# Kernel optimization log

Hardware: AMD Instinct MI355X
Metric: run time of the kernel (lower is better)

## Reference

```python
import jax, jax.numpy as jnp
import numpy as np

NUM_ITERATIONS = 10


def _nearest_neighbor(src, tgt):
    # src: [B,N,3], tgt: [B,M,3] -> indices [B,N] of nearest tgt point per src point
    inner = -2.0 * jnp.einsum('bnd,bmd->bnm', src, tgt)            # [B,N,M]
    xx = jnp.sum(src * src, axis=2, keepdims=True)                  # [B,N,1]
    yy = jnp.sum(tgt * tgt, axis=2, keepdims=True).transpose(0, 2, 1)  # [B,1,M]
    distances = xx + inner + yy                                     # [B,N,M]
    return jnp.argmin(distances, axis=2)                            # [B,N]


def _compute_transformation(src, tgt):
    # src, tgt: [B,N,3] matched pairs -> rigid (R [B,3,3], t [B,3])
    N = src.shape[1]
    c_src = jnp.mean(src, axis=1, keepdims=True)                    # [B,1,3]
    c_tgt = jnp.mean(tgt, axis=1, keepdims=True)                    # [B,1,3]
    H = jnp.einsum('bnd,bne->bde', src - c_src, tgt - c_tgt) / N    # [B,3,3]
    U, S, Vh = jnp.linalg.svd(H, full_matrices=False)
    V = jnp.swapaxes(Vh, -1, -2)                                    # matches torch.svd's V
    R = V @ jnp.swapaxes(U, -1, -2)
    det = jnp.linalg.det(R)                                         # [B]
    sign = 1.0 - 2.0 * (det < 0).astype(src.dtype)                  # +1 or -1
    # torch code scales V[:, :, 2] (third column of V)
    V = V * jnp.concatenate([jnp.ones_like(sign)[:, None],
                             jnp.ones_like(sign)[:, None],
                             sign[:, None]], axis=1)[:, None, :]    # scale col 2
    R = V @ jnp.swapaxes(U, -1, -2)                                 # [B,3,3]
    t = c_tgt[:, 0, :] - jnp.einsum('bij,bj->bi', R, c_src[:, 0, :])  # [B,3]
    return R, t


def _icp(src, tgt):
    transformed_src = src
    R = None
    t = None
    for _ in range(NUM_ITERATIONS):
        indices = _nearest_neighbor(transformed_src, tgt)           # [B,N]
        matched_tgt = jnp.take_along_axis(tgt, indices[:, :, None], axis=1)  # [B,N,3]
        R, t = _compute_transformation(transformed_src, matched_tgt)
        # faithful to torch: x @ R + t (R applied on the right)
        transformed_src = jnp.einsum('bnd,bde->bne', transformed_src, R) + t[:, None, :]
    return R, t, transformed_src


def setup_inputs() -> dict:
    key = jax.random.key(0)
    k1, k2 = jax.random.split(key)
    src = jax.random.normal(k1, (4, 4096, 3), dtype=jnp.float32)
    tgt = jax.random.normal(k2, (4, 4096, 3), dtype=jnp.float32)
    return {"src": src, "tgt": tgt}


def reference(src, tgt):
    # Returns (est_R [B,3,3], est_t [B,3], transformed_source [B,N,3])
    return _icp(src, tgt)
```

## Files before the change

kernel.cpp:

```cpp
#include <hip/hip_runtime.h>
#include <math.h>

#define NB 4
#define NP 4096
#define MP 4096

typedef __bf16 bf16x8 __attribute__((ext_vector_type(8)));
typedef float  f32x16 __attribute__((ext_vector_type(16)));

static __device__ __forceinline__ unsigned short bh(float f) {
    unsigned u = __float_as_uint(f);
    unsigned r = (u + 0x7FFFu + ((u >> 16) & 1u)) >> 16;
    return (unsigned short)r;
}
static __device__ __forceinline__ float hf(unsigned short h) {
    return __uint_as_float(((unsigned)h) << 16);
}

static __device__ __forceinline__ float frcp(float x)  { return __builtin_amdgcn_rcpf(x); }
static __device__ __forceinline__ float frsq(float x)  { return __builtin_amdgcn_rsqf(x); }
static __device__ __forceinline__ float fsqrt(float x) { return __builtin_amdgcn_sqrtf(x); }

__device__ __forceinline__ void kabsch_f32(const float* s, float* RtL) {
    const float invN = 1.0f / (float)NP;
    float cs[3] = { s[0] * invN, s[1] * invN, s[2] * invN };
    float ct[3] = { s[3] * invN, s[4] * invN, s[5] * invN };
    float H[3][3];
    for (int d = 0; d < 3; ++d)
        for (int e = 0; e < 3; ++e)
            H[d][e] = s[6 + d * 3 + e] * invN - cs[d] * ct[e];

    float A[3][3];
    for (int i = 0; i < 3; ++i)
        for (int j = 0; j < 3; ++j)
            A[i][j] = H[0][i] * H[0][j] + H[1][i] * H[1][j] + H[2][i] * H[2][j];

    float V[3][3] = {{1, 0, 0}, {0, 1, 0}, {0, 0, 1}};
    for (int sweep = 0; sweep < 6; ++sweep) {
        float off = A[0][1] * A[0][1] + A[0][2] * A[0][2] + A[1][2] * A[1][2];
        if (off < 1e-16f) break;
        for (int pi = 0; pi < 3; ++pi) {
            const int p = (pi == 2) ? 1 : 0;
            const int q = (pi == 0) ? 1 : 2;
            float apq = A[p][q];
            if (fabsf(apq) < 1e-30f) continue;
            float theta = (A[q][q] - A[p][p]) * 0.5f * frcp(apq);
            float t = frcp(fabsf(theta) + fsqrt(1.0f + theta * theta));
            if (theta < 0.0f) t = -t;
            float cth = frsq(1.0f + t * t);
            float sth = t * cth;
            float App = A[p][p], Aqq = A[q][q];
            A[p][p] = App - t * apq;
            A[q][q] = Aqq + t * apq;
            A[p][q] = A[q][p] = 0.0f;
            const int r = 3 - p - q;
            float Apr = A[p][r], Aqr = A[q][r];
            A[p][r] = A[r][p] = cth * Apr - sth * Aqr;
            A[q][r] = A[r][q] = sth * Apr + cth * Aqr;
            for (int i = 0; i < 3; ++i) {
                float Vip = V[i][p], Viq = V[i][q];
                V[i][p] = cth * Vip - sth * Viq;
                V[i][q] = sth * Vip + cth * Viq;
            }
        }
    }
    float lam[3] = { A[0][0], A[1][1], A[2][2] };
    for (int i = 0; i < 2; ++i)
        for (int j = i + 1; j < 3; ++j)
            if (lam[j] > lam[i]) {
                float tl = lam[i]; lam[i] = lam[j]; lam[j] = tl;
                for (int k = 0; k < 3; ++k) {
                    float tv = V[k][i]; V[k][i] = V[k][j]; V[k][j] = tv;
                }
            }

    float U[3][3];
    for (int k = 0; k < 3; ++k) {
        float w0 = H[0][0] * V[0][k] + H[0][1] * V[1][k] + H[0][2] * V[2][k];
        float w1 = H[1][0] * V[0][k] + H[1][1] * V[1][k] + H[1][2] * V[2][k];
        float w2 = H[2][0] * V[0][k] + H[2][1] * V[1][k] + H[2][2] * V[2][k];
        float d2 = w0 * w0 + w1 * w1 + w2 * w2;
        if (d2 > 1e-40f) {
            float inr = frsq(d2);
            U[0][k] = w0 * inr; U[1][k] = w1 * inr; U[2][k] = w2 * inr;
        } else {
            U[0][k] = U[1][0] * U[2][1] - U[2][0] * U[1][1];
            U[1][k] = U[2][0] * U[0][1] - U[0][0] * U[2][1];
            U[2][k] = U[0][0] * U[1][1] - U[1][0] * U[0][1];
        }
    }

    float detH = H[0][0] * (H[1][1] * H[2][2] - H[1][2] * H[2][1])
               - H[0][1] * (H[1][0] * H[2][2] - H[1][2] * H[2][0])
               + H[0][2] * (H[1][0] * H[2][1] - H[1][1] * H[2][0]);
    float sgn = (detH < 0.0f) ? -1.0f : 1.0f;

    float R[3][3];
    for (int i = 0; i < 3; ++i)
        for (int j = 0; j < 3; ++j)
            R[i][j] = V[i][0] * U[j][0] + V[i][1] * U[j][1] + sgn * V[i][2] * U[j][2];
    float tv[3];
    for (int i = 0; i < 3; ++i)
        tv[i] = ct[i] - (R[i][0] * cs[0] + R[i][1] * cs[1] + R[i][2] * cs[2]);

    for (int i = 0; i < 3; ++i)
        for (int j = 0; j < 3; ++j)
            RtL[i * 3 + j] = R[i][j];
    for (int i = 0; i < 3; ++i) RtL[9 + i] = tv[i];
}

__global__ __launch_bounds__(256) void icp_init(const float* __restrict__ tgt,
                                                float4* __restrict__ tgt4,
                                                uint4* __restrict__ Bbuf) {
    const int t    = blockIdx.x * 256 + threadIdx.x;
    const int b    = t >> 13;
    const int rem  = t & 8191;
    const int tile = rem >> 6;
    const int lane = rem & 63;
    const int n    = lane & 31;
    const int h    = lane >> 5;
    const int gt   = b * MP + tile * 32 + n;

    float x = tgt[gt * 3 + 0];
    float y = tgt[gt * 3 + 1];
    float z = tgt[gt * 3 + 2];
    float wv = x * x + y * y + z * z;

    unsigned short xh = bh(x), xl = bh(x - hf(xh));
    unsigned short yh = bh(y), yl = bh(y - hf(yh));
    unsigned short zh = bh(z), zl = bh(z - hf(zh));
    unsigned short wh = bh(wv), wl = bh(wv - hf(wh));
    const unsigned short ONE = 0x3F80;

    unsigned short s0, s1, s2, s3, s4, s5, s6, s7;
    if (h == 0) { s0 = xh; s1 = xh; s2 = xl; s3 = xl;
                  s4 = yh; s5 = yh; s6 = yl; s7 = yl; }
    else        { s0 = zh; s1 = zh; s2 = zl; s3 = zl;
                  s4 = wh; s5 = wl; s6 = ONE; s7 = ONE; }
    uint4 u;
    u.x = (unsigned)s0 | ((unsigned)s1 << 16);
    u.y = (unsigned)s2 | ((unsigned)s3 << 16);
    u.z = (unsigned)s4 | ((unsigned)s5 << 16);
    u.w = (unsigned)s6 | ((unsigned)s7 << 16);
    Bbuf[t] = u;

    if (h == 0) tgt4[gt] = make_float4(x, y, z, wv);
}

__global__ __launch_bounds__(1024, 4) void icp_scan(
        const float* __restrict__ src,
        const float4* __restrict__ tgt4,
        const uint4* __restrict__ Bbuf,
        float* __restrict__ S,
        const float* __restrict__ pprev,
        float* __restrict__ pout,
        int first) {
    __shared__ unsigned CK[512];
    __shared__ float RtL[12];

    const int blk = blockIdx.x;
    const int b   = blk >> 6;
    const int g   = blk & 63;
    const int tid = threadIdx.x;
    const int w   = tid >> 6;
    const int l   = tid & 63;
    const int ts  = w & 1;
    const int tr  = w >> 1;
    const int gsrc = b * NP + g * 64 + l;

    const uint4* Bw = Bbuf + (b * 128 + tr * 16) * 64;
    uint4 fb[4];
    fb[0] = Bw[l];
    fb[1] = Bw[64 + l];
    fb[2] = Bw[128 + l];
    fb[3] = Bw[192 + l];

    const float* P = first ? src : S;
    float x0 = P[gsrc * 3 + 0];
    float y0 = P[gsrc * 3 + 1];
    float z0 = P[gsrc * 3 + 2];

    if (w == 0) {
        if (first) {
            if (l < 12) RtL[l] = (l == 0 || l == 4 || l == 8) ? 1.0f : 0.0f;
        } else {
            const float4* rp = (const float4*)(pprev + (b * 64 + l) * 16);
            float4 r0 = rp[0], r1 = rp[1], r2 = rp[2], r3 = rp[3];
            float sm[15] = { r0.x, r0.y, r0.z, r0.w, r1.x, r1.y, r1.z, r1.w,
                             r2.x, r2.y, r2.z, r2.w, r3.x, r3.y, r3.z };
            #pragma unroll
            for (int k = 0; k < 15; ++k) {
                float v = sm[k];
                v += __shfl_down(v, 32);
                v += __shfl_down(v, 16);
                v += __shfl_down(v, 8);
                v += __shfl_down(v, 4);
                v += __shfl_down(v, 2);
                v += __shfl_down(v, 1);
                sm[k] = v;
            }
            if (l == 0) kabsch_f32(sm, RtL);
        }
    }
    __syncthreads();

    float px = x0 * RtL[0] + y0 * RtL[3] + z0 * RtL[6] + RtL[9];
    float py = x0 * RtL[1] + y0 * RtL[4] + z0 * RtL[7] + RtL[10];
    float pz = x0 * RtL[2] + y0 * RtL[5] + z0 * RtL[8] + RtL[11];
    if (w == 1) {
        S[gsrc * 3 + 0] = px;
        S[gsrc * 3 + 1] = py;
        S[gsrc * 3 + 2] = pz;
    }

    const int h = l >> 5;
    union { unsigned short s[8]; bf16x8 v; } Af;
    {
        const int j3 = ts * 32 + (l & 31);
        float pxj = __shfl(px, j3);
        float pyj = __shfl(py, j3);
        float pzj = __shfl(pz, j3);
        float ax = -2.0f * pxj, ay = -2.0f * pyj, az = -2.0f * pzj;
        float qv = pxj * pxj + pyj * pyj + pzj * pzj + 1.0f;
        unsigned short axh = bh(ax), axl = bh(ax - hf(axh));
        unsigned short ayh = bh(ay), ayl = bh(ay - hf(ayh));
        unsigned short azh = bh(az), azl = bh(az - hf(azh));
        unsigned short qh  = bh(qv), ql  = bh(qv - hf(qh));
        const unsigned short ONE = 0x3F80;
        if (h == 0) {
            Af.s[0] = axh; Af.s[1] = axl; Af.s[2] = axh; Af.s[3] = axl;
            Af.s[4] = ayh; Af.s[5] = ayl; Af.s[6] = ayh; Af.s[7] = ayl;
        } else {
            Af.s[0] = azh; Af.s[1] = azl; Af.s[2] = azh; Af.s[3] = azl;
            Af.s[4] = ONE; Af.s[5] = ONE; Af.s[6] = qh;  Af.s[7] = ql;
        }
    }

    f32x16 zero;
    #pragma unroll
    for (int i = 0; i < 16; ++i) zero[i] = 0.0f;

    float best[16];
    #pragma unroll
    for (int r = 0; r < 16; ++r) best[r] = __uint_as_float(0x7F7FFFFFu);

    const int col = l & 31;

    #pragma unroll
    for (int t = 0; t < 16; ++t) {
        bf16x8 Bf = __builtin_bit_cast(bf16x8, fb[t & 3]);
        if (t < 12) fb[t & 3] = Bw[(t + 4) * 64 + l];
        f32x16 d16 = __builtin_amdgcn_mfma_f32_32x32x16_bf16(Af.v, Bf, zero,
                                                             0, 0, 0);
        const unsigned idxk = (unsigned)((tr * 16 + t) * 32 + col);
        #pragma unroll
        for (int r = 0; r < 16; ++r) {
            float key = __uint_as_float(
                (__float_as_uint(d16[r]) & 0xFFFFF000u) | idxk);
            best[r] = fminf(best[r], key);
        }
    }

    #pragma unroll
    for (int r = 0; r < 16; ++r) {
        float v = best[r];
        v = fminf(v, __shfl_xor(v, 1));
        v = fminf(v, __shfl_xor(v, 2));
        v = fminf(v, __shfl_xor(v, 4));
        v = fminf(v, __shfl_xor(v, 8));
        v = fminf(v, __shfl_xor(v, 16));
        best[r] = v;
    }
    if ((l & 31) == 0) {
        #pragma unroll
        for (int r = 0; r < 16; ++r) {
            const int row = (r & 3) + 8 * (r >> 2) + 4 * h;
            CK[tr * 64 + ts * 32 + row] = __float_as_uint(best[r]);
        }
    }
    __syncthreads();

    if (w == 0) {
        unsigned kb = CK[l];
        #pragma unroll
        for (int k = 1; k < 8; ++k) {
            unsigned kk = CK[k * 64 + l];
            kb = kk < kb ? kk : kb;
        }
        const int idx = kb & 0xFFF;
        float4 mt = tgt4[b * MP + idx];
        const float tx = mt.x, ty = mt.y, tz = mt.z;

        float v[15];
        v[0]  = px;      v[1]  = py;      v[2]  = pz;
        v[3]  = tx;      v[4]  = ty;      v[5]  = tz;
        v[6]  = px * tx; v[7]  = px * ty; v[8]  = px * tz;
        v[9]  = py * tx; v[10] = py * ty; v[11] = py * tz;
        v[12] = pz * tx; v[13] = pz * ty; v[14] = pz * tz;
        #pragma unroll
        for (int k = 0; k < 15; ++k) {
            float s = v[k];
            s += __shfl_down(s, 32);
            s += __shfl_down(s, 16);
            s += __shfl_down(s, 8);
            s += __shfl_down(s, 4);
            s += __shfl_down(s, 2);
            s += __shfl_down(s, 1);
            v[k] = s;
        }
        if (l == 0) {
            float* pp = pout + blk * 16;
            #pragma unroll
            for (int k = 0; k < 15; ++k) pp[k] = v[k];
        }
    }
}

__global__ __launch_bounds__(256) void icp_final(
        const float* __restrict__ S,
        const float* __restrict__ plast,
        float* __restrict__ out) {
    __shared__ float RtL[12];
    const int bk  = blockIdx.x;
    const int tid = threadIdx.x;
    const int gid = bk * 256 + tid;
    const int b   = gid >> 12;

    if (tid < 64) {
        const float4* rp = (const float4*)(plast + (b * 64 + tid) * 16);
        float4 r0 = rp[0], r1 = rp[1], r2 = rp[2], r3 = rp[3];
        float sm[15] = { r0.x, r0.y, r0.z, r0.w, r1.x, r1.y, r1.z, r1.w,
                         r2.x, r2.y, r2.z, r2.w, r3.x, r3.y, r3.z };
        #pragma unroll
        for (int k = 0; k < 15; ++k) {
            float v = sm[k];
            v += __shfl_down(v, 32);
            v += __shfl_down(v, 16);
            v += __shfl_down(v, 8);
            v += __shfl_down(v, 4);
            v += __shfl_down(v, 2);
            v += __shfl_down(v, 1);
            sm[k] = v;
        }
        if (tid == 0) kabsch_f32(sm, RtL);
    }
    __syncthreads();

    float x = S[gid * 3 + 0];
    float y = S[gid * 3 + 1];
    float z = S[gid * 3 + 2];
    out[48 + gid * 3 + 0] = x * RtL[0] + y * RtL[3] + z * RtL[6] + RtL[9];
    out[48 + gid * 3 + 1] = x * RtL[1] + y * RtL[4] + z * RtL[7] + RtL[10];
    out[48 + gid * 3 + 2] = x * RtL[2] + y * RtL[5] + z * RtL[8] + RtL[11];
    if ((bk & 15) == 0) {
        if (tid < 9) out[b * 9 + tid] = RtL[tid];
        if (tid < 3) out[36 + b * 3 + tid] = RtL[9 + tid];
    }
}

extern "C" void kernel_launch(void* const* d_in, const int* in_sizes, int n_in,
                              void* d_out, int out_size, void* d_ws, size_t ws_size,
                              hipStream_t stream) {
    const float* src = (const float*)d_in[0];
    const float* tgt = (const float*)d_in[1];
    float* out = (float*)d_out;

    float* W     = (float*)d_ws;
    float4* tgt4 = (float4*)W;
    uint4*  Bbuf = (uint4*)(W + 65536);
    float*  S    = W + 65536 + 131072;
    float*  pA   = S + 49152;
    float*  pB   = pA + 4096;
    float* bufs[2] = { pA, pB };

    icp_init<<<128, 256, 0, stream>>>(tgt, tgt4, Bbuf);
    for (int k = 0; k < 10; ++k) {
        icp_scan<<<256, 1024, 0, stream>>>(src, tgt4, Bbuf, S,
                                           bufs[(k + 1) & 1], bufs[k & 1],
                                           k == 0 ? 1 : 0);
    }
    icp_final<<<64, 256, 0, stream>>>(S, bufs[1], out);
}
```

Baseline: 173.5 us.

## Split scan into 512 blocks of 32 source points each with 8 warps

Measured after the change: 199.2 us. +14.8%, slower.

```diff
diff --git a/kernel.cpp b/kernel.cpp
--- a/kernel.cpp
+++ b/kernel.cpp
@@ -147,7 +147,7 @@
     if (h == 0) tgt4[gt] = make_float4(x, y, z, wv);
 }
 
-__global__ __launch_bounds__(1024, 4) void icp_scan(
+__global__ __launch_bounds__(512, 4) void icp_scan(
         const float* __restrict__ src,
         const float4* __restrict__ tgt4,
         const uint4* __restrict__ Bbuf,
@@ -155,20 +155,20 @@
         const float* __restrict__ pprev,
         float* __restrict__ pout,
         int first) {
-    __shared__ unsigned CK[512];
+    __shared__ unsigned CK[256];
     __shared__ float RtL[12];
 
     const int blk = blockIdx.x;
-    const int b   = blk >> 6;
-    const int g   = blk & 63;
+    const int b   = blk >> 7;
+    const int g   = blk & 127;
     const int tid = threadIdx.x;
     const int w   = tid >> 6;
     const int l   = tid & 63;
-    const int ts  = w & 1;
-    const int tr  = w >> 1;
-    const int gsrc = b * NP + g * 64 + l;
-
-    const uint4* Bw = Bbuf + (b * 128 + tr * 16) * 64;
+    const int m   = l & 31;
+    const int h   = l >> 5;
+    const int gsrc = b * NP + g * 32 + m;
+
+    const uint4* Bw = Bbuf + (b * 128 + w * 16) * 64;
     uint4 fb[4];
     fb[0] = Bw[l];
     fb[1] = Bw[64 + l];
@@ -184,10 +184,14 @@
         if (first) {
             if (l < 12) RtL[l] = (l == 0 || l == 4 || l == 8) ? 1.0f : 0.0f;
         } else {
-            const float4* rp = (const float4*)(pprev + (b * 64 + l) * 16);
-            float4 r0 = rp[0], r1 = rp[1], r2 = rp[2], r3 = rp[3];
-            float sm[15] = { r0.x, r0.y, r0.z, r0.w, r1.x, r1.y, r1.z, r1.w,
-                             r2.x, r2.y, r2.z, r2.w, r3.x, r3.y, r3.z };
+            const float4* rp0 = (const float4*)(pprev + (b * 128 + l) * 16);
+            const float4* rp1 = (const float4*)(pprev + (b * 128 + 64 + l) * 16);
+            float4 a0 = rp0[0], a1 = rp0[1], a2 = rp0[2], a3 = rp0[3];
+            float4 c0 = rp1[0], c1 = rp1[1], c2 = rp1[2], c3 = rp1[3];
+            float sm[15] = { a0.x + c0.x, a0.y + c0.y, a0.z + c0.z, a0.w + c0.w,
+                             a1.x + c1.x, a1.y + c1.y, a1.z + c1.z, a1.w + c1.w,
+                             a2.x + c2.x, a2.y + c2.y, a2.z + c2.z, a2.w + c2.w,
+                             a3.x + c3.x, a3.y + c3.y, a3.z + c3.z };
             #pragma unroll
             for (int k = 0; k < 15; ++k) {
                 float v = sm[k];
@@ -207,21 +211,16 @@
     float px = x0 * RtL[0] + y0 * RtL[3] + z0 * RtL[6] + RtL[9];
     float py = x0 * RtL[1] + y0 * RtL[4] + z0 * RtL[7] + RtL[10];
     float pz = x0 * RtL[2] + y0 * RtL[5] + z0 * RtL[8] + RtL[11];
-    if (w == 1) {
+    if (w == 1 && h == 0) {
         S[gsrc * 3 + 0] = px;
         S[gsrc * 3 + 1] = py;
         S[gsrc * 3 + 2] = pz;
     }
 
-    const int h = l >> 5;
     union { unsigned short s[8]; bf16x8 v; } Af;
     {
-        const int j3 = ts * 32 + (l & 31);
-        float pxj = __shfl(px, j3);
-        float pyj = __shfl(py, j3);
-        float pzj = __shfl(pz, j3);
-        float ax = -2.0f * pxj, ay = -2.0f * pyj, az = -2.0f * pzj;
-        float qv = pxj * pxj + pyj * pyj + pzj * pzj + 1.0f;
+        float ax = -2.0f * px, ay = -2.0f * py, az = -2.0f * pz;
+        float qv = px * px + py * py + pz * pz + 1.0f;
         unsigned short axh = bh(ax), axl = bh(ax - hf(axh));
         unsigned short ayh = bh(ay), ayl = bh(ay - hf(ayh));
         unsigned short azh = bh(az), azl = bh(az - hf(azh));
@@ -244,15 +243,13 @@
     #pragma unroll
     for (int r = 0; r < 16; ++r) best[r] = __uint_as_float(0x7F7FFFFFu);
 
-    const int col = l & 31;
-
     #pragma unroll
     for (int t = 0; t < 16; ++t) {
         bf16x8 Bf = __builtin_bit_cast(bf16x8, fb[t & 3]);
         if (t < 12) fb[t & 3] = Bw[(t + 4) * 64 + l];
         f32x16 d16 = __builtin_amdgcn_mfma_f32_32x32x16_bf16(Af.v, Bf, zero,
                                                              0, 0, 0);
-        const unsigned idxk = (unsigned)((tr * 16 + t) * 32 + col);
+        const unsigned idxk = (unsigned)((w * 16 + t) * 32 + m);
         #pragma unroll
         for (int r = 0; r < 16; ++r) {
             float key = __uint_as_float(
@@ -271,32 +268,35 @@
         v = fminf(v, __shfl_xor(v, 16));
         best[r] = v;
     }
-    if ((l & 31) == 0) {
+    if (m == 0) {
         #pragma unroll
         for (int r = 0; r < 16; ++r) {
             const int row = (r & 3) + 8 * (r >> 2) + 4 * h;
-            CK[tr * 64 + ts * 32 + row] = __float_as_uint(best[r]);
+            CK[w * 32 + row] = __float_as_uint(best[r]);
         }
     }
     __syncthreads();
 
     if (w == 0) {
-        unsigned kb = CK[l];
-        #pragma unroll
-        for (int k = 1; k < 8; ++k) {
-            unsigned kk = CK[k * 64 + l];
-            kb = kk < kb ? kk : kb;
-        }
-        const int idx = kb & 0xFFF;
-        float4 mt = tgt4[b * MP + idx];
-        const float tx = mt.x, ty = mt.y, tz = mt.z;
-
         float v[15];
-        v[0]  = px;      v[1]  = py;      v[2]  = pz;
-        v[3]  = tx;      v[4]  = ty;      v[5]  = tz;
-        v[6]  = px * tx; v[7]  = px * ty; v[8]  = px * tz;
-        v[9]  = py * tx; v[10] = py * ty; v[11] = py * tz;
-        v[12] = pz * tx; v[13] = pz * ty; v[14] = pz * tz;
+        #pragma unroll
+        for (int k = 0; k < 15; ++k) v[k] = 0.0f;
+        if (l < 32) {
+            unsigned kb = CK[l];
+            #pragma unroll
+            for (int k = 1; k < 8; ++k) {
+                unsigned kk = CK[k * 32 + l];
+                kb = kk < kb ? kk : kb;
+            }
+            const int idx = kb & 0xFFF;
+            float4 mt = tgt4[b * MP + idx];
+            const float tx = mt.x, ty = mt.y, tz = mt.z;
+            v[0]  = px;      v[1]  = py;      v[2]  = pz;
+            v[3]  = tx;      v[4]  = ty;      v[5]  = tz;
+            v[6]  = px * tx; v[7]  = px * ty; v[8]  = px * tz;
+            v[9]  = py * tx; v[10] = py * ty; v[11] = py * tz;
+            v[12] = pz * tx; v[13] = pz * ty; v[14] = pz * tz;
+        }
         #pragma unroll
         for (int k = 0; k < 15; ++k) {
             float s = v[k];
@@ -327,10 +327,14 @@
     const int b   = gid >> 12;
 
     if (tid < 64) {
-        const float4* rp = (const float4*)(plast + (b * 64 + tid) * 16);
-        float4 r0 = rp[0], r1 = rp[1], r2 = rp[2], r3 = rp[3];
-        float sm[15] = { r0.x, r0.y, r0.z, r0.w, r1.x, r1.y, r1.z, r1.w,
-                         r2.x, r2.y, r2.z, r2.w, r3.x, r3.y, r3.z };
+        const float4* rp0 = (const float4*)(plast + (b * 128 + tid) * 16);
+        const float4* rp1 = (const float4*)(plast + (b * 128 + 64 + tid) * 16);
+        float4 a0 = rp0[0], a1 = rp0[1], a2 = rp0[2], a3 = rp0[3];
+        float4 c0 = rp1[0], c1 = rp1[1], c2 = rp1[2], c3 = rp1[3];
+        float sm[15] = { a0.x + c0.x, a0.y + c0.y, a0.z + c0.z, a0.w + c0.w,
+                         a1.x + c1.x, a1.y + c1.y, a1.z + c1.z, a1.w + c1.w,
+                         a2.x + c2.x, a2.y + c2.y, a2.z + c2.z, a2.w + c2.w,
+                         a3.x + c3.x, a3.y + c3.y, a3.z + c3.z };
         #pragma unroll
         for (int k = 0; k < 15; ++k) {
             float v = sm[k];
@@ -370,14 +374,14 @@
     uint4*  Bbuf = (uint4*)(W + 65536);
     float*  S    = W + 65536 + 131072;
     float*  pA   = S + 49152;
-    float*  pB   = pA + 4096;
+    float*  pB   = pA + 8192;
     float* bufs[2] = { pA, pB };
 
     icp_init<<<128, 256, 0, stream>>>(tgt, tgt4, Bbuf);
     for (int k = 0; k < 10; ++k) {
-        icp_scan<<<256, 1024, 0, stream>>>(src, tgt4, Bbuf, S,
-                                           bufs[(k + 1) & 1], bufs[k & 1],
-                                           k == 0 ? 1 : 0);
+        icp_scan<<<512, 512, 0, stream>>>(src, tgt4, Bbuf, S,
+                                          bufs[(k + 1) & 1], bufs[k & 1],
+                                          k == 0 ? 1 : 0);
     }
     icp_final<<<64, 256, 0, stream>>>(S, bufs[1], out);
 }
```
